# Optimization experiments

Hardware: AMD Instinct MI355X
Metric: run time of the kernel (lower is better)

The kernel has to match this reference:

```python
import jax, jax.numpy as jnp
import numpy as np

DIM = 128
HEADS = 8
RBF_K = 16
N_LIG = 20000
N_PROT = 80000
E = 262144
HEAD_DIM = DIM // HEADS
SCALE = HEAD_DIM ** -0.5


def setup_inputs() -> dict:
    key = jax.random.key(0)
    ks = jax.random.split(key, 16)
    inp = {
        "ligand_x": jax.random.normal(ks[0], (N_LIG, DIM), dtype=jnp.float32),
        "protein_x": jax.random.normal(ks[1], (N_PROT, DIM), dtype=jnp.float32),
        "cross_edges": jax.random.randint(ks[2], (E, 2), 0, N_LIG, dtype=jnp.int64)
        if jax.config.jax_enable_x64 else jax.random.randint(ks[2], (E, 2), 0, N_LIG, dtype=jnp.int32),
        "cross_attr": jax.random.uniform(ks[3], (E, RBF_K), dtype=jnp.float32),
        "Wq": jax.random.normal(ks[4], (DIM, DIM), dtype=jnp.float32) * (DIM ** -0.5),
        "bq": jax.random.normal(ks[5], (DIM,), dtype=jnp.float32) * 0.02,
        "Wk": jax.random.normal(ks[6], (DIM, DIM), dtype=jnp.float32) * (DIM ** -0.5),
        "bk": jax.random.normal(ks[7], (DIM,), dtype=jnp.float32) * 0.02,
        "Wv": jax.random.normal(ks[8], (DIM, DIM), dtype=jnp.float32) * (DIM ** -0.5),
        "bv": jax.random.normal(ks[9], (DIM,), dtype=jnp.float32) * 0.02,
        "Wo": jax.random.normal(ks[10], (DIM, DIM), dtype=jnp.float32) * (DIM ** -0.5),
        "bo": jax.random.normal(ks[11], (DIM,), dtype=jnp.float32) * 0.02,
        "Wr": jax.random.normal(ks[12], (RBF_K, HEADS), dtype=jnp.float32) * (RBF_K ** -0.5),
        "br": jax.random.normal(ks[13], (HEADS,), dtype=jnp.float32) * 0.02,
        "lig_start": 0,
        "prot_start": 0,
    }
    return inp


def _heads(t):
    return t.reshape(t.shape[0], HEADS, HEAD_DIM)


def _cross_attend(q_nodes, k_nodes, v_nodes, dst_idx, src_idx, rbf_bias, n_dst):
    # gather per-edge q/k/v: [E, H, D]
    qe = q_nodes[dst_idx]
    ke = k_nodes[src_idx]
    ve = v_nodes[src_idx]
    logits = jnp.einsum("ehd,ehd->eh", qe, ke) * SCALE + rbf_bias  # [E, H]
    # segment softmax over edges grouped by destination node
    m = jax.ops.segment_max(logits, dst_idx, num_segments=n_dst)  # [N, H]
    ex = jnp.exp(logits - m[dst_idx])
    s = jax.ops.segment_sum(ex, dst_idx, num_segments=n_dst)  # [N, H]
    w = ex / (s[dst_idx] + 1e-8)  # [E, H]
    agg = jax.ops.segment_sum(w[:, :, None] * ve, dst_idx, num_segments=n_dst)
    return agg.reshape(n_dst, HEADS * HEAD_DIM)


def reference(ligand_x, protein_x, cross_edges, cross_attr, Wq, bq, Wk, bk, Wv, bv,
              Wo, bo, Wr, br, lig_start, prot_start):
    n_lig, n_prot = ligand_x.shape[0], protein_x.shape[0]
    q_l = _heads(ligand_x @ Wq + bq)
    k_p = _heads(protein_x @ Wk + bk)
    v_p = _heads(protein_x @ Wv + bv)
    q_p = _heads(protein_x @ Wq + bq)
    k_l = _heads(ligand_x @ Wk + bk)
    v_l = _heads(ligand_x @ Wv + bv)

    lig_local = cross_edges[:, 0] - lig_start
    prot_local = cross_edges[:, 1] - prot_start
    rbf_bias = cross_attr @ Wr + br  # [E, heads]

    lig_agg = _cross_attend(q_l, k_p, v_p, lig_local, prot_local, rbf_bias, n_lig)
    prot_agg = _cross_attend(q_p, k_l, v_l, prot_local, lig_local, rbf_bias, n_prot)

    ligand_out = lig_agg @ Wo + bo   # dropout is identity at inference
    protein_out = prot_agg @ Wo + bo
    return (ligand_out, protein_out)
```

## Files before the change

kernel.cpp:

```cpp
#include <hip/hip_runtime.h>
#include <hip/hip_bf16.h>

typedef unsigned short u16;
typedef __attribute__((ext_vector_type(8))) short short8;
typedef __attribute__((ext_vector_type(4))) float f32x4;

__device__ __forceinline__ float bf2f(u16 u){
  union { unsigned int i; float f; } c; c.i = ((unsigned int)u) << 16; return c.f;
}
__device__ __forceinline__ u16 f2bf(float f){
  union { float f; unsigned int i; } c; c.f = f;
  unsigned int x = c.i;
  return (u16)((x + 0x7FFFu + ((x >> 16) & 1u)) >> 16);
}

__device__ __forceinline__ int edge_get(const int* __restrict__ e32, int i64, int e, int c){
  int idx = 2 * e + c;
  return i64 ? e32[2 * idx] : e32[idx];
}

__global__ __launch_bounds__(256) void init_all(
    const void* __restrict__ Wq, const void* __restrict__ Wk,
    const void* __restrict__ Wv, const void* __restrict__ Wo,
    const void* __restrict__ bq, const void* __restrict__ bk,
    const void* __restrict__ bv, const void* __restrict__ bo,
    u16* __restrict__ Wt, float* __restrict__ biasP,
    const u16* __restrict__ lig16, const int* __restrict__ e32,
    int* __restrict__ flags, int* __restrict__ desc,
    int* __restrict__ cnt, int ntot)
{
  int bx = blockIdx.x, tid = threadIdx.x;

  if (bx < 4){
    __shared__ int Fsh;
    if (tid < 64){
      int c = 0;
      #pragma unroll
      for (int j = 0; j < 4; j++){
        u16 u = lig16[(tid * 4 + j) * 2];
        int ex = (u >> 7) & 0xFF;
        if (ex >= 96 && ex < 160) c++;
      }
      #pragma unroll
      for (int off = 1; off < 64; off <<= 1) c += __shfl_xor(c, off);
      if (tid == 0) Fsh = (c < 128) ? 1 : 0;
    }
    __syncthreads();
    int F = Fsh;
    int mat = bx;
    const void* W = (mat == 0) ? Wq : (mat == 1) ? Wk : (mat == 2) ? Wv : Wo;
    const void* b = (mat == 0) ? bq : (mat == 1) ? bk : (mat == 2) ? bv : bo;
    u16* dst = Wt + mat * 16384;
    #pragma unroll 4
    for (int j = 0; j < 64; j++){
      int idx = tid + j * 256;
      u16 w = F ? f2bf(((const float*)W)[idx]) : ((const u16*)W)[idx];
      dst[(idx & 127) * 128 + (idx >> 7)] = w;
    }
    if (tid < 128)
      biasP[mat * 128 + tid] = F ? ((const float*)b)[tid] : bf2f(((const u16*)b)[tid]);
  } else if (bx == 4){
    if (tid < 64){
      int c = 0, nz = 0;
      #pragma unroll
      for (int j = 0; j < 4; j++){
        u16 u = lig16[(tid * 4 + j) * 2];
        int ex = (u >> 7) & 0xFF;
        if (ex >= 96 && ex < 160) c++;
        if (e32[(tid * 4 + j) * 2 + 1] != 0) nz++;
      }
      #pragma unroll
      for (int off = 1; off < 64; off <<= 1){
        c  += __shfl_xor(c, off);
        nz += __shfl_xor(nz, off);
      }
      if (tid == 0){
        flags[0] = (c < 128) ? 1 : 0;
        flags[1] = (nz == 0) ? 1 : 0;
      }
    }
    desc[tid] = 0;
    desc[256 + tid] = 0;
  } else {
    int i = (bx - 5) * 256 + tid;
    if (i < ntot) cnt[i] = 0;
  }
}

__global__ __launch_bounds__(256) void edge_pre(
    const void* __restrict__ attr, const void* __restrict__ Wr,
    const void* __restrict__ br, float* __restrict__ ebias,
    const int* __restrict__ edges, const int* __restrict__ ls_p,
    const int* __restrict__ ps_p, int* __restrict__ cnt, int nlig, int E_,
    const int* __restrict__ flags)
{
  __shared__ float w[16][8];
  __shared__ float b[8];
  int tid = threadIdx.x;
  int F = flags[0];
  if (tid < 128) w[tid >> 3][tid & 7] = F ? ((const float*)Wr)[tid] : bf2f(((const u16*)Wr)[tid]);
  if (tid < 8)   b[tid] = F ? ((const float*)br)[tid] : bf2f(((const u16*)br)[tid]);
  __syncthreads();
  int e = blockIdx.x * 256 + tid;
  if (e >= E_) return;

  int I64 = flags[1];
  int dl = edge_get(edges, I64, e, 0) - ls_p[0];
  int dp = edge_get(edges, I64, e, 1) - ps_p[0];
  atomicAdd(&cnt[dl], 1);
  atomicAdd(&cnt[nlig + dp], 1);

  float a[16];
  if (F){
    const float* af = (const float*)attr;
    #pragma unroll
    for (int j = 0; j < 4; j++){
      float4 t = *(const float4*)&af[e * 16 + j * 4];
      a[4*j] = t.x; a[4*j+1] = t.y; a[4*j+2] = t.z; a[4*j+3] = t.w;
    }
  } else {
    const u16* au = (const u16*)attr;
    #pragma unroll
    for (int j = 0; j < 4; j++){
      ushort4 t = *(const ushort4*)&au[e * 16 + j * 4];
      a[4*j] = bf2f(t.x); a[4*j+1] = bf2f(t.y); a[4*j+2] = bf2f(t.z); a[4*j+3] = bf2f(t.w);
    }
  }
  #pragma unroll
  for (int hh = 0; hh < 8; hh++){
    float s = b[hh];
    #pragma unroll
    for (int r = 0; r < 16; r++) s += a[r] * w[r][hh];
    ebias[e * 8 + hh] = s;
  }
}

__global__ __launch_bounds__(256) void scan_lookback(
    const int* __restrict__ cnt, int* __restrict__ offs, int* __restrict__ cursor,
    int* __restrict__ desc, int n)
{
  __shared__ int lds[256];
  __shared__ int base_s;
  int bx = blockIdx.x, tid = threadIdx.x;
  int i0 = bx * 2048 + tid * 8;

  int v[8]; int s = 0;
  #pragma unroll
  for (int j = 0; j < 8; j++){
    int idx = i0 + j;
    v[j] = (idx < n) ? cnt[idx] : 0;
    s += v[j];
  }
  lds[tid] = s; __syncthreads();
  for (int off = 1; off < 256; off <<= 1){
    int t = (tid >= off) ? lds[tid - off] : 0;
    __syncthreads();
    lds[tid] += t;
    __syncthreads();
  }
  int thr_excl = lds[tid] - s;
  int block_sum = lds[255];

  if (tid == 0){
    if (bx == 0){
      __hip_atomic_store(&desc[0], (block_sum << 2) | 2, __ATOMIC_RELEASE,
                         __HIP_MEMORY_SCOPE_AGENT);
      base_s = 0;
    } else {
      __hip_atomic_store(&desc[bx], (block_sum << 2) | 1, __ATOMIC_RELEASE,
                         __HIP_MEMORY_SCOPE_AGENT);
      int running = 0;
      int idx = bx - 1;
      while (true){
        int d;
        while (((d = __hip_atomic_load(&desc[idx], __ATOMIC_ACQUIRE,
                                       __HIP_MEMORY_SCOPE_AGENT)) & 3) == 0){
          __builtin_amdgcn_s_sleep(1);
        }
        running += (d >> 2);
        if ((d & 3) == 2) break;
        idx--;
      }
      __hip_atomic_store(&desc[bx], ((running + block_sum) << 2) | 2,
                         __ATOMIC_RELEASE, __HIP_MEMORY_SCOPE_AGENT);
      base_s = running;
    }
  }
  __syncthreads();

  int base = base_s + thr_excl;
  #pragma unroll
  for (int j = 0; j < 8; j++){
    int idx = i0 + j;
    if (idx < n){
      offs[idx] = base;
      cursor[idx] = base;
      base += v[j];
      if (idx == n - 1) offs[n] = base;
    }
  }
}

__global__ __launch_bounds__(256) void fat_qkv_sc(
    const void* __restrict__ A0, int M0, const void* __restrict__ A1, int M1, int mb0,
    const u16* __restrict__ Wt, const float* __restrict__ biasP,
    u16* __restrict__ O0b, u16* __restrict__ O1b, u16* __restrict__ O2b,
    const int* __restrict__ offs,
    const int* __restrict__ edges, const int* __restrict__ ls_p,
    const int* __restrict__ ps_p, int* __restrict__ cursor,
    int2* __restrict__ sorted, int nlig, int E_, const int* __restrict__ flags)
{
  __shared__ __align__(16) char smem[34816];
  int tid = threadIdx.x;
  int F = flags[0];

  int TT = mb0 + ((M1 + 63) >> 6);
  int eb = (E_ + 255) >> 8;
  int G  = TT + eb;
  int bx = blockIdx.x;
  long long pp = (long long)bx * TT;
  int tile = (int)(pp / G);
  int isQ  = (int)(((long long)(bx + 1) * TT) / G) > tile;

  if (isQ){
    u16 (*As)[136] = (u16(*)[136])smem;
    u16 (*Fs)[136] = (u16(*)[136])(smem + 17408);
    __shared__ int act;
    int AF = F;
    const void* A; int M, m0, orow;
    if (tile < mb0){ A = A0; M = M0; m0 = tile * 64;          orow = m0; }
    else           { A = A1; M = M1; m0 = (tile - mb0) * 64;  orow = M0 + m0; }

    if (tid == 0) act = 0;
    __syncthreads();
    if (tid < 64 && m0 + tid < M){
      int r = orow + tid;
      if (offs[r + 1] > offs[r]) act = 1;
    }
    __syncthreads();
    if (!act) return;

    if (AF){
      const float* Af = (const float*)A;
      #pragma unroll
      for (int j = 0; j < 8; j++){
        int u = tid + j * 256, row = u >> 5, c4 = (u & 31) * 4;
        float4 v = make_float4(0.f, 0.f, 0.f, 0.f);
        if (m0 + row < M) v = *(const float4*)&Af[(size_t)(m0 + row) * 128 + c4];
        ushort4 o; o.x = f2bf(v.x); o.y = f2bf(v.y); o.z = f2bf(v.z); o.w = f2bf(v.w);
        *(ushort4*)&As[row][c4] = o;
      }
    } else {
      const float4* Au = (const float4*)A;
      #pragma unroll
      for (int j = 0; j < 4; j++){
        int u = tid + j * 256, row = u >> 4, c8 = (u & 15);
        float4 v = make_float4(0.f, 0.f, 0.f, 0.f);
        if (m0 + row < M) v = Au[(size_t)(m0 + row) * 16 + c8];
        *(float4*)&As[row][c8 * 8] = v;
      }
    }
    __syncthreads();

    int wave = tid >> 6, lane = tid & 63;
    int quad = lane >> 4, ml = lane & 15;

    for (int mat = 0; mat < 3; mat++){
      const u16* wp = Wt + (size_t)mat * 16384
                        + (size_t)(wave * 32 + ml) * 128 + quad * 8;
      short8 wf0[4], wf1[4];
      #pragma unroll
      for (int kk = 0; kk < 4; kk++){
        wf0[kk] = *(const short8*)&wp[kk * 32];
        wf1[kk] = *(const short8*)&wp[2048 + kk * 32];
      }
      float b0 = biasP[mat * 128 + wave * 32 + ml];
      float b1 = biasP[mat * 128 + wave * 32 + 16 + ml];

      f32x4 acc[4][2];
      #pragma unroll
      for (int mt = 0; mt < 4; mt++){
        acc[mt][0] = (f32x4){0.f, 0.f, 0.f, 0.f};
        acc[mt][1] = (f32x4){0.f, 0.f, 0.f, 0.f};
      }
      #pragma unroll
      for (int mt = 0; mt < 4; mt++){
        #pragma unroll
        for (int kk = 0; kk < 4; kk++){
          short8 af = *(const short8*)&As[mt * 16 + ml][kk * 32 + quad * 8];
          acc[mt][0] = __builtin_amdgcn_mfma_f32_16x16x32_bf16(af, wf0[kk], acc[mt][0], 0, 0, 0);
          acc[mt][1] = __builtin_amdgcn_mfma_f32_16x16x32_bf16(af, wf1[kk], acc[mt][1], 0, 0, 0);
        }
      }

      if (mat > 0) __syncthreads();
      #pragma unroll
      for (int mt = 0; mt < 4; mt++){
        #pragma unroll
        for (int r = 0; r < 4; r++){
          int row = mt * 16 + quad * 4 + r;
          Fs[row][wave * 32 + ml]      = f2bf(acc[mt][0][r] + b0);
          Fs[row][wave * 32 + 16 + ml] = f2bf(acc[mt][1][r] + b1);
        }
      }
      __syncthreads();
      u16* Cb = (mat == 0) ? O0b : ((mat == 1) ? O1b : O2b);
      #pragma unroll
      for (int j = 0; j < 4; j++){
        int u = tid + j * 256, row = u >> 4, c8 = (u & 15) * 8;
        if (m0 + row < M)
          *(short8*)&Cb[(size_t)(orow + row) * 128 + c8] = *(const short8*)&Fs[row][c8];
      }
    }
  } else {
    int eidx = bx - tile;
    int e = eidx * 256 + tid;
    if (e >= E_) return;
    int I64 = flags[1];
    int dl = edge_get(edges, I64, e, 0) - ls_p[0];
    int dp = edge_get(edges, I64, e, 1) - ps_p[0];
    int p1 = atomicAdd(&cursor[dl], 1);        sorted[p1] = make_int2(e, nlig + dp);
    int p2 = atomicAdd(&cursor[nlig + dp], 1); sorted[p2] = make_int2(e, dl);
  }
}

__global__ __launch_bounds__(256) void attn_kernel(
    const u16* __restrict__ Q, const u16* __restrict__ K, const u16* __restrict__ V,
    const int2* __restrict__ sorted, const int* __restrict__ offs,
    const float* __restrict__ ebias, u16* __restrict__ AGG, int ntot)
{
  int t = blockIdx.x * 4 + (threadIdx.x >> 6);
  if (t >= ntot) return;
  int lane = threadIdx.x & 63;
  int ql = lane & 15;
  int q4 = lane >> 4;
  int h  = ql >> 1;

  int beg = offs[t], end = offs[t + 1];

  if (beg == end){
    if (lane < 16){
      short8 z = {0, 0, 0, 0, 0, 0, 0, 0};
      *(short8*)&AGG[(size_t)t * 128 + ql * 8] = z;
    }
    return;
  }

  short8 qv = *(const short8*)&Q[(size_t)t * 128 + ql * 8];
  float qf[8];
  #pragma unroll
  for (int j = 0; j < 8; j++) qf[j] = bf2f((u16)qv[j]);

  float m = -1e30f, l = 0.f;
  float a[8];
  #pragma unroll
  for (int j = 0; j < 8; j++) a[j] = 0.f;

  int i = beg + q4;
  int2 cur = make_int2(0, 0), nxt = make_int2(0, 0);
  if (i < end)     cur = sorted[i];
  if (i + 4 < end) nxt = sorted[i + 4];

  short8 kA = {0,0,0,0,0,0,0,0}, vA = {0,0,0,0,0,0,0,0};
  float ebA = 0.f;
  if (i < end){
    kA = *(const short8*)&K[(size_t)cur.y * 128 + ql * 8];
    vA = *(const short8*)&V[(size_t)cur.y * 128 + ql * 8];
    ebA = ebias[(size_t)cur.x * 8 + h];
  }

  while (i < end){
    short8 kB = {0,0,0,0,0,0,0,0}, vB = {0,0,0,0,0,0,0,0};
    float ebB = 0.f;
    if (i + 4 < end){
      kB = *(const short8*)&K[(size_t)nxt.y * 128 + ql * 8];
      vB = *(const short8*)&V[(size_t)nxt.y * 128 + ql * 8];
      ebB = ebias[(size_t)nxt.x * 8 + h];
    }
    int2 n2 = make_int2(0, 0);
    if (i + 8 < end) n2 = sorted[i + 8];

    float s = 0.f;
    #pragma unroll
    for (int j = 0; j < 8; j++) s += qf[j] * bf2f((u16)kA[j]);
    s += __shfl_xor(s, 1);
    float logit = s * 0.25f + ebA;
    float nm = fmaxf(m, logit);
    float alpha = __expf(m - nm);
    float p = __expf(logit - nm);
    #pragma unroll
    for (int j = 0; j < 8; j++) a[j] = a[j] * alpha + p * bf2f((u16)vA[j]);
    l = l * alpha + p;
    m = nm;

    kA = kB; vA = vB; ebA = ebB;
    cur = nxt; nxt = n2;
    i += 4;
  }

  #pragma unroll
  for (int mask = 16; mask <= 32; mask <<= 1){
    float mo = __shfl_xor(m, mask);
    float lo = __shfl_xor(l, mask);
    float nm = fmaxf(m, mo);
    float sA = __expf(m - nm);
    float sB = __expf(mo - nm);
    l = l * sA + lo * sB;
    #pragma unroll
    for (int j = 0; j < 8; j++){
      float ao = __shfl_xor(a[j], mask);
      a[j] = a[j] * sA + ao * sB;
    }
    m = nm;
  }

  if (lane < 16){
    float inv = 1.f / (l + 1e-8f);
    short8 o;
    #pragma unroll
    for (int j = 0; j < 8; j++) o[j] = (short)f2bf(a[j] * inv);
    *(short8*)&AGG[(size_t)t * 128 + ql * 8] = o;
  }
}

__global__ __launch_bounds__(256) void out_proj(
    const u16* __restrict__ AGG, int M, const u16* __restrict__ Wt,
    const float* __restrict__ biasP, void* __restrict__ OUT,
    const int* __restrict__ offs, const int* __restrict__ flags)
{
  __shared__ __align__(16) u16 As[64][136];
  __shared__ __align__(16) u16 Fs[64][136];
  __shared__ int act;

  int tid = threadIdx.x;
  int F = flags[0];
  int m0 = blockIdx.x * 64;

  if (tid == 0) act = 0;
  __syncthreads();
  if (tid < 64 && m0 + tid < M){
    if (offs[m0 + tid + 1] > offs[m0 + tid]) act = 1;
  }
  __syncthreads();

  if (!act){
    if (F){
      float* Of = (float*)OUT;
      #pragma unroll
      for (int j = 0; j < 8; j++){
        int u = tid + j * 256, row = u >> 5, c4 = (u & 31) * 4;
        if (m0 + row < M)
          *(float4*)&Of[(size_t)(m0 + row) * 128 + c4] = *(const float4*)&biasP[384 + c4];
      }
    } else {
      u16* Ob = (u16*)OUT;
      #pragma unroll
      for (int j = 0; j < 4; j++){
        int u = tid + j * 256, row = u >> 4, c8 = (u & 15) * 8;
        if (m0 + row < M){
          short8 s8;
          #pragma unroll
          for (int k = 0; k < 8; k++) s8[k] = (short)f2bf(biasP[384 + c8 + k]);
          *(short8*)&Ob[(size_t)(m0 + row) * 128 + c8] = s8;
        }
      }
    }
    return;
  }

  {
    const float4* Au = (const float4*)AGG;
    #pragma unroll
    for (int j = 0; j < 4; j++){
      int u = tid + j * 256, row = u >> 4, c8 = (u & 15);
      float4 v = make_float4(0.f, 0.f, 0.f, 0.f);
      if (m0 + row < M) v = Au[(size_t)(m0 + row) * 16 + c8];
      *(float4*)&As[row][c8 * 8] = v;
    }
  }
  __syncthreads();

  int wave = tid >> 6, lane = tid & 63;
  int quad = lane >> 4, ml = lane & 15;

  const u16* wp = Wt + (size_t)3 * 16384 + (size_t)(wave * 32 + ml) * 128 + quad * 8;
  short8 wf0[4], wf1[4];
  #pragma unroll
  for (int kk = 0; kk < 4; kk++){
    wf0[kk] = *(const short8*)&wp[kk * 32];
    wf1[kk] = *(const short8*)&wp[2048 + kk * 32];
  }
  float b0 = biasP[384 + wave * 32 + ml];
  float b1 = biasP[384 + wave * 32 + 16 + ml];

  f32x4 acc[4][2];
  #pragma unroll
  for (int mt = 0; mt < 4; mt++){
    acc[mt][0] = (f32x4){0.f, 0.f, 0.f, 0.f};
    acc[mt][1] = (f32x4){0.f, 0.f, 0.f, 0.f};
  }
  #pragma unroll
  for (int mt = 0; mt < 4; mt++){
    #pragma unroll
    for (int kk = 0; kk < 4; kk++){
      short8 af = *(const short8*)&As[mt * 16 + ml][kk * 32 + quad * 8];
      acc[mt][0] = __builtin_amdgcn_mfma_f32_16x16x32_bf16(af, wf0[kk], acc[mt][0], 0, 0, 0);
      acc[mt][1] = __builtin_amdgcn_mfma_f32_16x16x32_bf16(af, wf1[kk], acc[mt][1], 0, 0, 0);
    }
  }

  if (F){
    float* Of = (float*)OUT;
    #pragma unroll
    for (int mt = 0; mt < 4; mt++){
      #pragma unroll
      for (int r = 0; r < 4; r++){
        int row = mt * 16 + quad * 4 + r;
        if (m0 + row < M){
          float* op = &Of[(size_t)(m0 + row) * 128 + wave * 32 + ml];
          op[0]  = acc[mt][0][r] + b0;
          op[16] = acc[mt][1][r] + b1;
        }
      }
    }
  } else {
    #pragma unroll
    for (int mt = 0; mt < 4; mt++){
      #pragma unroll
      for (int r = 0; r < 4; r++){
        int row = mt * 16 + quad * 4 + r;
        Fs[row][wave * 32 + ml]      = f2bf(acc[mt][0][r] + b0);
        Fs[row][wave * 32 + 16 + ml] = f2bf(acc[mt][1][r] + b1);
      }
    }
    __syncthreads();
    u16* Ob = (u16*)OUT;
    #pragma unroll
    for (int j = 0; j < 4; j++){
      int u = tid + j * 256, row = u >> 4, c8 = (u & 15) * 8;
      if (m0 + row < M)
        *(short8*)&Ob[(size_t)(m0 + row) * 128 + c8] = *(const short8*)&Fs[row][c8];
    }
  }
}

extern "C" void kernel_launch(void* const* d_in, const int* in_sizes, int n_in,
                              void* d_out, int out_size, void* d_ws, size_t ws_size,
                              hipStream_t stream)
{
  const void* ligand_x  = d_in[0];
  const void* protein_x = d_in[1];
  const int* edges      = (const int*)d_in[2];
  const void* attr      = d_in[3];
  const void* Wq = d_in[4];  const void* bq = d_in[5];
  const void* Wk = d_in[6];  const void* bk = d_in[7];
  const void* Wv = d_in[8];  const void* bv = d_in[9];
  const void* Wo = d_in[10]; const void* bo = d_in[11];
  const void* Wr = d_in[12]; const void* br = d_in[13];
  const int* ls_p = (const int*)d_in[14];
  const int* ps_p = (const int*)d_in[15];

  const int nlig = in_sizes[0] / 128;
  const int nprot = in_sizes[1] / 128;
  const int E = in_sizes[2] / 2;
  const int ntot = nlig + nprot;

  char* w = (char*)d_ws;
  size_t off = 0;
  auto alloc = [&](size_t bytes) -> void* {
    void* p = w + off;
    off = (off + bytes + 255) & ~(size_t)255;
    return p;
  };
  int*   flags = (int*)alloc(256);
  u16*   Wt    = (u16*)alloc(4 * 16384 * 2);
  float* biasP = (float*)alloc(4 * 128 * 4);
  u16* Qb  = (u16*)alloc((size_t)ntot * 128 * 2);
  u16* Kb  = (u16*)alloc((size_t)ntot * 128 * 2);
  u16* Vb  = (u16*)alloc((size_t)ntot * 128 * 2);
  u16* AGG = (u16*)alloc((size_t)ntot * 128 * 2);
  float* ebias = (float*)alloc((size_t)E * 8 * 4);
  int* cnt    = (int*)alloc((size_t)ntot * 4);
  int* offs   = (int*)alloc((size_t)(ntot + 1) * 4);
  int* cursor = (int*)alloc((size_t)ntot * 4);
  int* desc   = (int*)alloc(512 * 4);
  int2* sorted = (int2*)alloc((size_t)2 * E * 8);
  (void)ws_size; (void)n_in; (void)out_size;

  const int mb_l = (nlig + 63) / 64;
  const int mb_p = (nprot + 63) / 64;
  const int mb_t = (ntot + 63) / 64;
  const int eb = (E + 255) / 256;
  const int nb = (ntot + 255) / 256;
  const int nsb = (ntot + 2047) / 2048;

  init_all<<<nb + 5, 256, 0, stream>>>(
      Wq, Wk, Wv, Wo, bq, bk, bv, bo, Wt, biasP,
      (const u16*)ligand_x, edges, flags, desc, cnt, ntot);

  edge_pre<<<eb, 256, 0, stream>>>(attr, Wr, br, ebias, edges, ls_p, ps_p,
                                   cnt, nlig, E, flags);

  scan_lookback<<<nsb, 256, 0, stream>>>(cnt, offs, cursor, desc, ntot);

  const int TT = mb_l + mb_p;
  fat_qkv_sc<<<TT + eb, 256, 0, stream>>>(
      ligand_x, nlig, protein_x, nprot, mb_l,
      Wt, biasP, Qb, Kb, Vb,
      offs, edges, ls_p, ps_p, cursor, sorted, nlig, E, flags);

  attn_kernel<<<(ntot + 3) / 4, 256, 0, stream>>>(Qb, Kb, Vb, sorted, offs, ebias, AGG, ntot);

  out_proj<<<mb_t, 256, 0, stream>>>(AGG, ntot, Wt, biasP, d_out, offs, flags);
}
```

Baseline: 291.3 us.

## Pre-permute edge bias into destination-sorted order during scatter

Result: no change. 296.0 us (+1.6%).

```diff
diff --git a/kernel.cpp b/kernel.cpp
--- a/kernel.cpp
+++ b/kernel.cpp
@@ -205,10 +205,11 @@
     const void* __restrict__ A0, int M0, const void* __restrict__ A1, int M1, int mb0,
     const u16* __restrict__ Wt, const float* __restrict__ biasP,
     u16* __restrict__ O0b, u16* __restrict__ O1b, u16* __restrict__ O2b,
-    const int* __restrict__ offs,
+    const int* __restrict__ offs, const float* __restrict__ ebias,
     const int* __restrict__ edges, const int* __restrict__ ls_p,
     const int* __restrict__ ps_p, int* __restrict__ cursor,
-    int2* __restrict__ sorted, int nlig, int E_, const int* __restrict__ flags)
+    int* __restrict__ sSrc, float* __restrict__ sBias,
+    int nlig, int E_, const int* __restrict__ flags)
 {
   __shared__ __align__(16) char smem[34816];
   int tid = threadIdx.x;
@@ -319,15 +320,23 @@
     int I64 = flags[1];
     int dl = edge_get(edges, I64, e, 0) - ls_p[0];
     int dp = edge_get(edges, I64, e, 1) - ps_p[0];
-    int p1 = atomicAdd(&cursor[dl], 1);        sorted[p1] = make_int2(e, nlig + dp);
-    int p2 = atomicAdd(&cursor[nlig + dp], 1); sorted[p2] = make_int2(e, dl);
+    float4 eb0 = *(const float4*)&ebias[(size_t)e * 8];
+    float4 eb1 = *(const float4*)&ebias[(size_t)e * 8 + 4];
+    int p1 = atomicAdd(&cursor[dl], 1);
+    sSrc[p1] = nlig + dp;
+    *(float4*)&sBias[(size_t)p1 * 8]     = eb0;
+    *(float4*)&sBias[(size_t)p1 * 8 + 4] = eb1;
+    int p2 = atomicAdd(&cursor[nlig + dp], 1);
+    sSrc[p2] = dl;
+    *(float4*)&sBias[(size_t)p2 * 8]     = eb0;
+    *(float4*)&sBias[(size_t)p2 * 8 + 4] = eb1;
   }
 }
 
 __global__ __launch_bounds__(256) void attn_kernel(
     const u16* __restrict__ Q, const u16* __restrict__ K, const u16* __restrict__ V,
-    const int2* __restrict__ sorted, const int* __restrict__ offs,
-    const float* __restrict__ ebias, u16* __restrict__ AGG, int ntot)
+    const int* __restrict__ sSrc, const float* __restrict__ sBias,
+    const int* __restrict__ offs, u16* __restrict__ AGG, int ntot)
 {
   int t = blockIdx.x * 4 + (threadIdx.x >> 6);
   if (t >= ntot) return;
@@ -337,19 +346,12 @@
   int h  = ql >> 1;
 
   int beg = offs[t], end = offs[t + 1];
-
-  if (beg == end){
-    if (lane < 16){
-      short8 z = {0, 0, 0, 0, 0, 0, 0, 0};
-      *(short8*)&AGG[(size_t)t * 128 + ql * 8] = z;
-    }
-    return;
-  }
+  if (beg == end) return;
 
   short8 qv = *(const short8*)&Q[(size_t)t * 128 + ql * 8];
   float qf[8];
   #pragma unroll
-  for (int j = 0; j < 8; j++) qf[j] = bf2f((u16)qv[j]);
+  for (int j = 0; j < 8; j++) qf[j] = bf2f((u16)qv[j]) * 0.25f;
 
   float m = -1e30f, l = 0.f;
   float a[8];
@@ -357,34 +359,34 @@
   for (int j = 0; j < 8; j++) a[j] = 0.f;
 
   int i = beg + q4;
-  int2 cur = make_int2(0, 0), nxt = make_int2(0, 0);
-  if (i < end)     cur = sorted[i];
-  if (i + 4 < end) nxt = sorted[i + 4];
+  int cur = 0, nxt = 0;
+  if (i < end)     cur = sSrc[i];
+  if (i + 4 < end) nxt = sSrc[i + 4];
 
   short8 kA = {0,0,0,0,0,0,0,0}, vA = {0,0,0,0,0,0,0,0};
   float ebA = 0.f;
   if (i < end){
-    kA = *(const short8*)&K[(size_t)cur.y * 128 + ql * 8];
-    vA = *(const short8*)&V[(size_t)cur.y * 128 + ql * 8];
-    ebA = ebias[(size_t)cur.x * 8 + h];
+    kA = *(const short8*)&K[(size_t)cur * 128 + ql * 8];
+    vA = *(const short8*)&V[(size_t)cur * 128 + ql * 8];
+    ebA = sBias[(size_t)i * 8 + h];
   }
 
   while (i < end){
     short8 kB = {0,0,0,0,0,0,0,0}, vB = {0,0,0,0,0,0,0,0};
     float ebB = 0.f;
     if (i + 4 < end){
-      kB = *(const short8*)&K[(size_t)nxt.y * 128 + ql * 8];
-      vB = *(const short8*)&V[(size_t)nxt.y * 128 + ql * 8];
-      ebB = ebias[(size_t)nxt.x * 8 + h];
-    }
-    int2 n2 = make_int2(0, 0);
-    if (i + 8 < end) n2 = sorted[i + 8];
+      kB = *(const short8*)&K[(size_t)nxt * 128 + ql * 8];
+      vB = *(const short8*)&V[(size_t)nxt * 128 + ql * 8];
+      ebB = sBias[(size_t)(i + 4) * 8 + h];
+    }
+    int n2 = 0;
+    if (i + 8 < end) n2 = sSrc[i + 8];
 
     float s = 0.f;
     #pragma unroll
     for (int j = 0; j < 8; j++) s += qf[j] * bf2f((u16)kA[j]);
     s += __shfl_xor(s, 1);
-    float logit = s * 0.25f + ebA;
+    float logit = s + ebA;
     float nm = fmaxf(m, logit);
     float alpha = __expf(m - nm);
     float p = __expf(logit - nm);
@@ -431,6 +433,7 @@
   __shared__ __align__(16) u16 As[64][136];
   __shared__ __align__(16) u16 Fs[64][136];
   __shared__ int act;
+  __shared__ int actRow[64];
 
   int tid = threadIdx.x;
   int F = flags[0];
@@ -438,8 +441,11 @@
 
   if (tid == 0) act = 0;
   __syncthreads();
-  if (tid < 64 && m0 + tid < M){
-    if (offs[m0 + tid + 1] > offs[m0 + tid]) act = 1;
+  if (tid < 64){
+    int r = m0 + tid;
+    int a = (r < M) ? (offs[r + 1] > offs[r] ? 1 : 0) : 0;
+    actRow[tid] = a;
+    if (a) act = 1;
   }
   __syncthreads();
 
@@ -474,7 +480,7 @@
     for (int j = 0; j < 4; j++){
       int u = tid + j * 256, row = u >> 4, c8 = (u & 15);
       float4 v = make_float4(0.f, 0.f, 0.f, 0.f);
-      if (m0 + row < M) v = Au[(size_t)(m0 + row) * 16 + c8];
+      if (m0 + row < M && actRow[row]) v = Au[(size_t)(m0 + row) * 16 + c8];
       *(float4*)&As[row][c8 * 8] = v;
     }
   }
@@ -584,7 +590,8 @@
   int* offs   = (int*)alloc((size_t)(ntot + 1) * 4);
   int* cursor = (int*)alloc((size_t)ntot * 4);
   int* desc   = (int*)alloc(512 * 4);
-  int2* sorted = (int2*)alloc((size_t)2 * E * 8);
+  int*   sSrc  = (int*)alloc((size_t)2 * E * 4);
+  float* sBias = (float*)alloc((size_t)2 * E * 8 * 4);
   (void)ws_size; (void)n_in; (void)out_size;
 
   const int mb_l = (nlig + 63) / 64;
@@ -607,9 +614,10 @@
   fat_qkv_sc<<<TT + eb, 256, 0, stream>>>(
       ligand_x, nlig, protein_x, nprot, mb_l,
       Wt, biasP, Qb, Kb, Vb,
-      offs, edges, ls_p, ps_p, cursor, sorted, nlig, E, flags);
-
-  attn_kernel<<<(ntot + 3) / 4, 256, 0, stream>>>(Qb, Kb, Vb, sorted, offs, ebias, AGG, ntot);
+      offs, ebias, edges, ls_p, ps_p, cursor, sSrc, sBias, nlig, E, flags);
+
+  attn_kernel<<<(ntot + 3) / 4, 256, 0, stream>>>(
+      Qb, Kb, Vb, sSrc, sBias, offs, AGG, ntot);
 
   out_proj<<<mb_t, 256, 0, stream>>>(AGG, ntot, Wt, biasP, d_out, offs, flags);
 }
```
